# Kernel tuning notes

Hardware: AMD Instinct MI355X
Metric: run time of the kernel (lower is better)

The kernel has to match this reference:

```python
import jax, jax.numpy as jnp
import numpy as np

B, S, D = 4, 4096, 64   # batch, seq_len, input_size
H, HD = 4, 16           # num_heads, head_dim


def setup_inputs() -> dict:
    key = jax.random.key(0)
    ks = jax.random.split(key, 9)
    sd = 1.0 / np.sqrt(D)          # torch Linear default uniform(-1/sqrt(fan_in), ...)
    so = 1.0 / np.sqrt(H * HD)
    u = lambda k, shape, s: jax.random.uniform(k, shape, jnp.float32, -s, s)
    return {
        "x": jax.random.normal(ks[0], (B, S, D), jnp.float32),
        "Wq": u(ks[1], (H, D, HD), sd), "bq": u(ks[2], (H, HD), sd),
        "Wk": u(ks[3], (H, D, HD), sd), "bk": u(ks[4], (H, HD), sd),
        "Wv": u(ks[5], (H, D, HD), sd), "bv": u(ks[6], (H, HD), sd),
        "Wo": u(ks[7], (H * HD, D), so), "bo": u(ks[8], (D,), so),
    }


def reference(x, Wq, bq, Wk, bk, Wv, bv, Wo, bo):
    # Batched per-head projections (fuses the original per-head Linear loop)
    q = jnp.einsum('bsd,hde->bhse', x, Wq) + bq[None, :, None, :]
    k = jnp.einsum('bsd,hde->bhse', x, Wk) + bk[None, :, None, :]
    v = jnp.einsum('bsd,hde->bhse', x, Wv) + bv[None, :, None, :]
    # scores: [B, H, S(query), S(key)]
    scores = jnp.einsum('bhse,bhte->bhst', q, k) / np.sqrt(HD).astype(np.float32)
    # FAITHFUL quirk: torch Softmax(dim=1) on [B,S,S] normalizes over the QUERY axis
    w = jax.nn.softmax(scores, axis=2)
    attended = jnp.einsum('bhst,bhte->bhse', w, v)          # [B,H,S,HD]
    concat = attended.transpose(0, 2, 1, 3).reshape(B, S, H * HD)
    out = concat @ Wo + bo                                   # [B,S,D]
    # FAITHFUL quirk: final softmax over the sequence axis (dim=1)
    return jax.nn.softmax(out, axis=1)
```

## Files before the change

### kernel.cpp

```cpp
#include <hip/hip_runtime.h>
#include <hip/hip_bf16.h>


#define BB 4
#define SS 4096
#define DD 64
#define HH 4
#define HDD 16

typedef unsigned int u32;
typedef unsigned short u16;
typedef __attribute__((ext_vector_type(8))) short bfrag;
typedef __attribute__((ext_vector_type(4))) float floatx4;
typedef __attribute__((ext_vector_type(16))) float floatx16;
typedef __attribute__((ext_vector_type(2))) u32 u32x2;
typedef __attribute__((ext_vector_type(4))) u32 u32x4;

#define LOG2E 1.4426950408889634074f
#define QSCALE (LOG2E * 0.25f)

__device__ __forceinline__ float fexp2(float x) {
#if __has_builtin(__builtin_amdgcn_exp2f)
  return __builtin_amdgcn_exp2f(x);
#else
  float r; asm("v_exp_f32 %0, %1" : "=v"(r) : "v"(x)); return r;
#endif
}
__device__ __forceinline__ float frcp(float x) {
#if __has_builtin(__builtin_amdgcn_rcpf)
  return __builtin_amdgcn_rcpf(x);
#else
  float r; asm("v_rcp_f32 %0, %1" : "=v"(r) : "v"(x)); return r;
#endif
}

__device__ __forceinline__ u16 f2bf(float f) {
  u32 u = __builtin_bit_cast(u32, f);
  return (u16)((u + 0x7FFFu + ((u >> 16) & 1u)) >> 16);
}
__device__ __forceinline__ u32 pack_bf(float lo, float hi) {
#if __has_builtin(__builtin_amdgcn_perm)
  return __builtin_amdgcn_perm(__builtin_bit_cast(u32, hi),
                               __builtin_bit_cast(u32, lo), 0x07060302u);
#else
  u32 a = __builtin_bit_cast(u32, lo);
  u32 b = __builtin_bit_cast(u32, hi);
  return (a >> 16) | (b & 0xFFFF0000u);
#endif
}

__global__ __launch_bounds__(256) void k_proj(
    const float* __restrict__ x,
    const float* __restrict__ Wq, const float* __restrict__ bq,
    const float* __restrict__ Wk, const float* __restrict__ bk,
    const float* __restrict__ Wv, const float* __restrict__ bv,
    u16* __restrict__ qb, u16* __restrict__ kb, float* __restrict__ vf)
{
  __shared__ float xs[16 * 64];
  const int tid = threadIdx.x;
  const int blk = blockIdx.x;
  const int b   = blk >> 8;
  const int s0  = (blk & 255) << 4;
  ((float4*)xs)[tid] = ((const float4*)(x + ((size_t)b * SS + s0) * DD))[tid];
  __syncthreads();

  const int col = tid & 63, h = col >> 4, e = col & 15;
  const int rg  = tid >> 6;
  float aq[4] = {0,0,0,0}, ak[4] = {0,0,0,0}, av[4] = {0,0,0,0};
  const int wofs = h * (DD * HDD) + e;
#pragma unroll 4
  for (int d = 0; d < DD; ++d) {
    float wq = Wq[wofs + d * HDD];
    float wk = Wk[wofs + d * HDD];
    float wv = Wv[wofs + d * HDD];
    const float* xr = xs + (rg * 4) * 64 + d;
#pragma unroll
    for (int r = 0; r < 4; ++r) {
      float xv = xr[r * 64];
      aq[r] += xv * wq; ak[r] += xv * wk; av[r] += xv * wv;
    }
  }
  const float bqv = bq[col], bkv = bk[col], bvv = bv[col];
  size_t base = ((size_t)(b * HH + h) * SS + (s0 + rg * 4)) * HDD + e;
#pragma unroll
  for (int r = 0; r < 4; ++r) {
    qb[base + r * HDD] = f2bf((aq[r] + bqv) * QSCALE);
    kb[base + r * HDD] = f2bf(ak[r] + bkv);
    vf[base + r * HDD] = av[r] + bvv;
  }
}

__global__ __launch_bounds__(256, 8) void k_colsum(
    const u16* __restrict__ qb, const u16* __restrict__ kb,
    float* __restrict__ csp)
{
  const int tid = threadIdx.x;
  const int lane = tid & 63, w = tid >> 6;
  const int l31 = lane & 31, hl = lane >> 5;
  const int bh = blockIdx.z, chunk = blockIdx.y;
  const int t0 = blockIdx.x * 128 + w * 32;
  const size_t base = (size_t)bh * (SS * HDD);

  const bfrag kf = *(const bfrag*)(kb + base + (size_t)(t0 + l31) * HDD + hl * 8);
  const u16* qp = qb + base + (size_t)l31 * HDD + hl * 8;
  const floatx16 z16 = {0.f};
  float c0 = 0.f, c1 = 0.f, c2 = 0.f, c3 = 0.f;
  const int s0 = chunk * 1024;
#pragma unroll 2
  for (int s = s0; s < s0 + 1024; s += 32) {
    bfrag qfr = *(const bfrag*)(qp + (size_t)s * HDD);
    floatx16 d = __builtin_amdgcn_mfma_f32_32x32x16_bf16(qfr, kf, z16, 0, 0, 0);
#pragma unroll
    for (int i = 0; i < 4; ++i) {
      c0 += fexp2(d[4 * i + 0]);
      c1 += fexp2(d[4 * i + 1]);
      c2 += fexp2(d[4 * i + 2]);
      c3 += fexp2(d[4 * i + 3]);
    }
  }
  float c = (c0 + c1) + (c2 + c3);
  c += __shfl_xor(c, 32, 64);
  if (hl == 0)
    csp[((size_t)bh * 4 + chunk) * SS + t0 + l31] = c;
}

__global__ __launch_bounds__(256, 8) void k_attn(
    const u16* __restrict__ qb, const u16* __restrict__ kb,
    const float* __restrict__ vf, const float* __restrict__ csp,
    float* __restrict__ attp)
{
  __shared__ __align__(16) u16 vls[16][264];
  const int tid  = threadIdx.x;
  const int lane = tid & 63, w = tid >> 6;
  const int l31 = lane & 31, hl = lane >> 5;
  const int bh = blockIdx.z, b = bh >> 2, h = bh & 3;
  const int tq = blockIdx.y;
  const int s0 = blockIdx.x * 128 + w * 32;
  const size_t base = (size_t)bh * (SS * HDD);
  const int tbq = tq * 1024;

  const bfrag qf = *(const bfrag*)(qb + base + (size_t)(s0 + l31) * HDD + hl * 8);
  const u16* kp = kb + base + (size_t)l31 * HDD + hl * 8;
  const floatx16 z16 = {0.f};
  floatx16 acc = {0.f};

  const float4* vsrc = (const float4*)(vf + base + (size_t)tbq * HDD);
  const float* cspb = csp + (size_t)bh * 4 * SS + tbq;

#pragma unroll
  for (int ch = 0; ch < 4; ++ch) {
    __syncthreads();
#pragma unroll
    for (int kk = 0; kk < 4; ++kk) {
      int c = kk * 256 + tid;
      int tl = c >> 2, g = c & 3;
      float4 vv = vsrc[ch * 1024 + c];
      const float* cp = cspb + ch * 256 + tl;
      float rc = frcp(cp[0] + cp[SS] + cp[2 * SS] + cp[3 * SS]);
      int i5 = tl >> 5, t5 = tl & 31;
      int sub = ((t5 >> 2) & 1) * 16 + ((t5 >> 3) << 2) + (t5 & 3);
      u16* wp = &vls[0][0] + i5 * 32 + sub;
      wp[(4 * g + 0) * 264] = f2bf(vv.x * rc);
      wp[(4 * g + 1) * 264] = f2bf(vv.y * rc);
      wp[(4 * g + 2) * 264] = f2bf(vv.z * rc);
      wp[(4 * g + 3) * 264] = f2bf(vv.w * rc);
    }
    __syncthreads();

    const u16* vrow = &vls[0][0] + (l31 & 15) * 264 + hl * 16;
    const int tb = tbq + ch * 256;
#pragma unroll 2
    for (int it = 0; it < 8; ++it) {
      bfrag kf = *(const bfrag*)(kp + (size_t)(tb + it * 32) * HDD);
      floatx16 d = __builtin_amdgcn_mfma_f32_32x32x16_bf16(kf, qf, z16, 0, 0, 0);
      u32 wr[8];
#pragma unroll
      for (int p = 0; p < 8; ++p)
        wr[p] = pack_bf(fexp2(d[2 * p]), fexp2(d[2 * p + 1]));
      const u16* va = vrow + it * 32;
      u32x4 af0 = *(const u32x4*)(va);
      u32x4 af1 = *(const u32x4*)(va + 8);
      u32x4 ef0 = {wr[0], wr[1], wr[2], wr[3]};
      u32x4 ef1 = {wr[4], wr[5], wr[6], wr[7]};
      acc = __builtin_amdgcn_mfma_f32_32x32x16_bf16(
          __builtin_bit_cast(bfrag, af0), __builtin_bit_cast(bfrag, ef0), acc, 0, 0, 0);
      acc = __builtin_amdgcn_mfma_f32_32x32x16_bf16(
          __builtin_bit_cast(bfrag, af1), __builtin_bit_cast(bfrag, ef1), acc, 0, 0, 0);
    }
  }

  float* ao = attp + (((size_t)tq * BB + b) * SS + s0 + l31) * (HH * HDD)
            + h * HDD + 4 * hl;
  float4 lo4 = {acc[0], acc[1], acc[2], acc[3]};
  float4 hi4 = {acc[4], acc[5], acc[6], acc[7]};
  *(float4*)ao       = lo4;
  *(float4*)(ao + 8) = hi4;
}

__global__ __launch_bounds__(256) void k_oproj(
    const float* __restrict__ att, const float* __restrict__ Wo,
    const float* __restrict__ bo, float* __restrict__ outp,
    float* __restrict__ part)
{
  __shared__ float wols[64 * 64];
  __shared__ float red[4][64];
  const int tid = threadIdx.x;
  const int blk = blockIdx.x;
  const int b = blk >> 9, s0 = (blk & 511) << 3;
#pragma unroll
  for (int i = 0; i < 4; ++i)
    ((float4*)wols)[tid + 256 * i] = ((const float4*)Wo)[tid + 256 * i];
  __syncthreads();

  const int d = tid & 63, sg = tid >> 6;
  const float bov = bo[d];
  const size_t so = (size_t)BB * SS * 16;
  float es = 0.f;
#pragma unroll
  for (int r = 0; r < 2; ++r) {
    int s = s0 + sg * 2 + r;
    const floatx4* row = (const floatx4*)(att + ((size_t)b * SS + s) * 64);
    float acc = bov;
#pragma unroll
    for (int j = 0; j < 16; ++j) {
      floatx4 c = (row[j] + row[j + so]) + (row[j + 2 * so] + row[j + 3 * so]);
      acc += c[0] * wols[(4*j+0)*64 + d] + c[1] * wols[(4*j+1)*64 + d]
           + c[2] * wols[(4*j+2)*64 + d] + c[3] * wols[(4*j+3)*64 + d];
    }
    outp[((size_t)b * SS + s) * 64 + d] = acc;
    es += fexp2(acc * LOG2E);
  }
  red[sg][d] = es;
  __syncthreads();
  if (tid < 64)
    part[((size_t)b * 512 + (blk & 511)) * 64 + tid] =
        red[0][tid] + red[1][tid] + red[2][tid] + red[3][tid];
}

__global__ __launch_bounds__(256) void k_softmax(
    const float* __restrict__ outp, const float* __restrict__ part,
    float* __restrict__ out)
{
  __shared__ float red[4][64];
  __shared__ float rs[64];
  const int tid = threadIdx.x, d = tid & 63, sg = tid >> 6;
  const int st = blockIdx.x;
  const int b = blockIdx.y;
  {
    float e = 0.f;
    const float* pp = part + ((size_t)b * 512 + sg * 128) * 64 + d;
#pragma unroll 8
    for (int c = 0; c < 128; ++c) e += pp[c * 64];
    red[sg][d] = e;
  }
  __syncthreads();
  if (tid < 64)
    rs[tid] = frcp(red[0][tid] + red[1][tid] + red[2][tid] + red[3][tid]);
  __syncthreads();
  const float r = rs[d];
  const size_t rowbase = ((size_t)b * SS + st * 64 + sg * 16) * 64 + d;
#pragma unroll 4
  for (int i = 0; i < 16; ++i)
    out[rowbase + i * 64] = fexp2(outp[rowbase + i * 64] * LOG2E) * r;
}

extern "C" void kernel_launch(void* const* d_in, const int* in_sizes, int n_in,
                              void* d_out, int out_size, void* d_ws, size_t ws_size,
                              hipStream_t stream) {
  const float* x  = (const float*)d_in[0];
  const float* Wq = (const float*)d_in[1];
  const float* bq = (const float*)d_in[2];
  const float* Wk = (const float*)d_in[3];
  const float* bk = (const float*)d_in[4];
  const float* Wv = (const float*)d_in[5];
  const float* bv = (const float*)d_in[6];
  const float* Wo = (const float*)d_in[7];
  const float* bo = (const float*)d_in[8];

  char* ws = (char*)d_ws;
  constexpr size_t QB_OFF  = 0;
  constexpr size_t KB_OFF  = (size_t)2  << 20;
  constexpr size_t VF_OFF  = (size_t)4  << 20;
  constexpr size_t CSP_OFF = (size_t)10 << 20;
  constexpr size_t ATT_OFF = (size_t)11 << 20;
  constexpr size_t OUT_OFF = (size_t)27 << 20;
  constexpr size_t PT_OFF  = (size_t)31 << 20;

  u16*   qb   = (u16*)  (ws + QB_OFF);
  u16*   kb   = (u16*)  (ws + KB_OFF);
  float* vf   = (float*)(ws + VF_OFF);
  float* csp  = (float*)(ws + CSP_OFF);
  float* attp = (float*)(ws + ATT_OFF);
  float* outp = (float*)(ws + OUT_OFF);
  float* part = (float*)(ws + PT_OFF);
  float* out  = (float*)d_out;

  hipLaunchKernelGGL(k_proj,    dim3(1024),       dim3(256), 0, stream,
                     x, Wq, bq, Wk, bk, Wv, bv, qb, kb, vf);
  hipLaunchKernelGGL(k_colsum,  dim3(32, 4, 16),  dim3(256), 0, stream, qb, kb, csp);
  hipLaunchKernelGGL(k_attn,    dim3(32, 4, 16),  dim3(256), 0, stream,
                     qb, kb, vf, csp, attp);
  hipLaunchKernelGGL(k_oproj,   dim3(2048),       dim3(256), 0, stream,
                     attp, Wo, bo, outp, part);
  hipLaunchKernelGGL(k_softmax, dim3(64, 4),      dim3(256), 0, stream, outp, part, out);
}
```

Baseline: 209.3 us.

## Double-buffer V staging in LDS and prefetch next chunk during MFMA loop

The attention kernel now keeps two LDS buffers for the scaled V tile. It issues global loads for the next chunk's V and column-sum reciprocals before the MFMA loop and writes them to the alternate buffer afterwards, which drops one barrier per chunk. Each thread also now handles a whole key row: one reciprocal computation and four float4 loads, instead of four reciprocals for scattered rows. This aims to hide global load latency behind compute, at the cost of more LDS (which may limit occupancy at 8 blocks/CU) and more live registers for the prefetched data.

```diff
diff --git a/kernel.cpp b/kernel.cpp
--- a/kernel.cpp
+++ b/kernel.cpp
@@ -129,7 +129,7 @@
     const float* __restrict__ vf, const float* __restrict__ csp,
     float* __restrict__ attp)
 {
-  __shared__ __align__(16) u16 vls[16][264];
+  __shared__ __align__(16) u16 vls[2][16][264];
   const int tid  = threadIdx.x;
   const int lane = tid & 63, w = tid >> 6;
   const int l31 = lane & 31, hl = lane >> 5;
@@ -147,27 +147,39 @@
   const float4* vsrc = (const float4*)(vf + base + (size_t)tbq * HDD);
   const float* cspb = csp + (size_t)bh * 4 * SS + tbq;
 
+  const int t5 = tid & 31, i5 = tid >> 5;
+  const int sub = ((t5 >> 2) & 1) * 16 + ((t5 >> 3) << 2) + (t5 & 3);
+  const int wcol = i5 * 32 + sub;
+
+  float4 pv[4];
+  float rc;
+  {
+    const float* cp = cspb + tid;
+    rc = frcp(cp[0] + cp[SS] + cp[2 * SS] + cp[3 * SS]);
+#pragma unroll
+    for (int g = 0; g < 4; ++g) pv[g] = vsrc[tid * 4 + g];
+    u16* wp = &vls[0][0][0] + wcol;
+#pragma unroll
+    for (int g = 0; g < 4; ++g) {
+      wp[(4 * g + 0) * 264] = f2bf(pv[g].x * rc);
+      wp[(4 * g + 1) * 264] = f2bf(pv[g].y * rc);
+      wp[(4 * g + 2) * 264] = f2bf(pv[g].z * rc);
+      wp[(4 * g + 3) * 264] = f2bf(pv[g].w * rc);
+    }
+  }
+  __syncthreads();
+
 #pragma unroll
   for (int ch = 0; ch < 4; ++ch) {
-    __syncthreads();
-#pragma unroll
-    for (int kk = 0; kk < 4; ++kk) {
-      int c = kk * 256 + tid;
-      int tl = c >> 2, g = c & 3;
-      float4 vv = vsrc[ch * 1024 + c];
-      const float* cp = cspb + ch * 256 + tl;
-      float rc = frcp(cp[0] + cp[SS] + cp[2 * SS] + cp[3 * SS]);
-      int i5 = tl >> 5, t5 = tl & 31;
-      int sub = ((t5 >> 2) & 1) * 16 + ((t5 >> 3) << 2) + (t5 & 3);
-      u16* wp = &vls[0][0] + i5 * 32 + sub;
-      wp[(4 * g + 0) * 264] = f2bf(vv.x * rc);
-      wp[(4 * g + 1) * 264] = f2bf(vv.y * rc);
-      wp[(4 * g + 2) * 264] = f2bf(vv.z * rc);
-      wp[(4 * g + 3) * 264] = f2bf(vv.w * rc);
-    }
-    __syncthreads();
-
-    const u16* vrow = &vls[0][0] + (l31 & 15) * 264 + hl * 16;
+    if (ch < 3) {
+      const float* cp = cspb + (ch + 1) * 256 + tid;
+      rc = frcp(cp[0] + cp[SS] + cp[2 * SS] + cp[3 * SS]);
+#pragma unroll
+      for (int g = 0; g < 4; ++g)
+        pv[g] = vsrc[(ch + 1) * 1024 + tid * 4 + g];
+    }
+
+    const u16* vrow = &vls[ch & 1][0][0] + (l31 & 15) * 264 + hl * 16;
     const int tb = tbq + ch * 256;
 #pragma unroll 2
     for (int it = 0; it < 8; ++it) {
@@ -187,6 +199,18 @@
       acc = __builtin_amdgcn_mfma_f32_32x32x16_bf16(
           __builtin_bit_cast(bfrag, af1), __builtin_bit_cast(bfrag, ef1), acc, 0, 0, 0);
     }
+
+    if (ch < 3) {
+      u16* wp = &vls[(ch + 1) & 1][0][0] + wcol;
+#pragma unroll
+      for (int g = 0; g < 4; ++g) {
+        wp[(4 * g + 0) * 264] = f2bf(pv[g].x * rc);
+        wp[(4 * g + 1) * 264] = f2bf(pv[g].y * rc);
+        wp[(4 * g + 2) * 264] = f2bf(pv[g].z * rc);
+        wp[(4 * g + 3) * 264] = f2bf(pv[g].w * rc);
+      }
+    }
+    __syncthreads();
   }
 
   float* ao = attp + (((size_t)tq * BB + b) * SS + s0 + l31) * (HH * HDD)
```

Result: no change. 211.8 us (+1.2%).

## Precompute bf16 transposed V and fold column-sum normalizer into MFMA accumulator

Applied to the files above, without the earlier changes.

Adds a k_prep kernel that converts V to bf16 in the permuted transposed layout once and computes -log2 of the per-key column sums. k_attn then seeds the score MFMA accumulator with that negative log, so exp2 yields already-normalized weights. It reads V straight from global memory instead of rebuilding a scaled LDS tile per chunk, which removes the __syncthreads, LDS traffic and redundant reciprocal work. The cost is an extra kernel launch and extra global reads of the normalizer per iteration. Normalized weights now go through bf16 instead of V*rc, which may slightly change rounding.

```diff
diff --git a/kernel.cpp b/kernel.cpp
--- a/kernel.cpp
+++ b/kernel.cpp
@@ -31,6 +31,13 @@
   return __builtin_amdgcn_rcpf(x);
 #else
   float r; asm("v_rcp_f32 %0, %1" : "=v"(r) : "v"(x)); return r;
+#endif
+}
+__device__ __forceinline__ float flog2(float x) {
+#if __has_builtin(__builtin_amdgcn_logf)
+  return __builtin_amdgcn_logf(x);
+#else
+  return __builtin_log2f(x);
 #endif
 }
 
@@ -124,12 +131,51 @@
     csp[((size_t)bh * 4 + chunk) * SS + t0 + l31] = c;
 }
 
+__global__ __launch_bounds__(256) void k_prep(
+    const float* __restrict__ vf, const float* __restrict__ csp,
+    u16* __restrict__ vt, float* __restrict__ nlcs)
+{
+  __shared__ u16 tile[16][264];
+  const int tid = threadIdx.x;
+  const int bh  = blockIdx.y;
+  const int t0  = blockIdx.x << 8;
+
+  {
+    const float* cp = csp + (size_t)bh * 4 * SS + t0 + tid;
+    float s = (cp[0] + cp[SS]) + (cp[2 * SS] + cp[3 * SS]);
+    nlcs[(size_t)bh * SS + t0 + tid] = -flog2(s);
+  }
+
+  {
+    const int t5 = tid & 31, i5 = tid >> 5;
+    const int sub = ((t5 >> 2) & 1) * 16 + ((t5 >> 3) << 2) + (t5 & 3);
+    const int wcol = i5 * 32 + sub;
+    const floatx4* vsrc = (const floatx4*)(vf + ((size_t)bh * SS + t0 + tid) * HDD);
+#pragma unroll
+    for (int g = 0; g < 4; ++g) {
+      floatx4 vv = vsrc[g];
+      tile[4 * g + 0][wcol] = f2bf(vv[0]);
+      tile[4 * g + 1][wcol] = f2bf(vv[1]);
+      tile[4 * g + 2][wcol] = f2bf(vv[2]);
+      tile[4 * g + 3][wcol] = f2bf(vv[3]);
+    }
+  }
+  __syncthreads();
+
+  {
+    const int row = tid >> 4, seg = tid & 15;
+    const u32x4* src = (const u32x4*)(&tile[row][seg * 16]);
+    u32x4* dst = (u32x4*)(vt + ((size_t)bh * HDD + row) * SS + t0 + seg * 16);
+    dst[0] = src[0];
+    dst[1] = src[1];
+  }
+}
+
 __global__ __launch_bounds__(256, 8) void k_attn(
     const u16* __restrict__ qb, const u16* __restrict__ kb,
-    const float* __restrict__ vf, const float* __restrict__ csp,
+    const u16* __restrict__ vt, const float* __restrict__ nlcs,
     float* __restrict__ attp)
 {
-  __shared__ __align__(16) u16 vls[16][264];
   const int tid  = threadIdx.x;
   const int lane = tid & 63, w = tid >> 6;
   const int l31 = lane & 31, hl = lane >> 5;
@@ -140,53 +186,34 @@
   const int tbq = tq * 1024;
 
   const bfrag qf = *(const bfrag*)(qb + base + (size_t)(s0 + l31) * HDD + hl * 8);
-  const u16* kp = kb + base + (size_t)l31 * HDD + hl * 8;
-  const floatx16 z16 = {0.f};
+  const u16* kp = kb + base + (size_t)(tbq + l31) * HDD + hl * 8;
+  const u16* vrow = vt + ((size_t)bh * HDD + (l31 & 15)) * SS + tbq + hl * 16;
+  const float4* np4 = (const float4*)(nlcs + (size_t)bh * SS + tbq + 4 * hl);
+
   floatx16 acc = {0.f};
 
-  const float4* vsrc = (const float4*)(vf + base + (size_t)tbq * HDD);
-  const float* cspb = csp + (size_t)bh * 4 * SS + tbq;
-
-#pragma unroll
-  for (int ch = 0; ch < 4; ++ch) {
-    __syncthreads();
-#pragma unroll
-    for (int kk = 0; kk < 4; ++kk) {
-      int c = kk * 256 + tid;
-      int tl = c >> 2, g = c & 3;
-      float4 vv = vsrc[ch * 1024 + c];
-      const float* cp = cspb + ch * 256 + tl;
-      float rc = frcp(cp[0] + cp[SS] + cp[2 * SS] + cp[3 * SS]);
-      int i5 = tl >> 5, t5 = tl & 31;
-      int sub = ((t5 >> 2) & 1) * 16 + ((t5 >> 3) << 2) + (t5 & 3);
-      u16* wp = &vls[0][0] + i5 * 32 + sub;
-      wp[(4 * g + 0) * 264] = f2bf(vv.x * rc);
-      wp[(4 * g + 1) * 264] = f2bf(vv.y * rc);
-      wp[(4 * g + 2) * 264] = f2bf(vv.z * rc);
-      wp[(4 * g + 3) * 264] = f2bf(vv.w * rc);
-    }
-    __syncthreads();
-
-    const u16* vrow = &vls[0][0] + (l31 & 15) * 264 + hl * 16;
-    const int tb = tbq + ch * 256;
 #pragma unroll 2
-    for (int it = 0; it < 8; ++it) {
-      bfrag kf = *(const bfrag*)(kp + (size_t)(tb + it * 32) * HDD);
-      floatx16 d = __builtin_amdgcn_mfma_f32_32x32x16_bf16(kf, qf, z16, 0, 0, 0);
-      u32 wr[8];
-#pragma unroll
-      for (int p = 0; p < 8; ++p)
-        wr[p] = pack_bf(fexp2(d[2 * p]), fexp2(d[2 * p + 1]));
-      const u16* va = vrow + it * 32;
-      u32x4 af0 = *(const u32x4*)(va);
-      u32x4 af1 = *(const u32x4*)(va + 8);
-      u32x4 ef0 = {wr[0], wr[1], wr[2], wr[3]};
-      u32x4 ef1 = {wr[4], wr[5], wr[6], wr[7]};
-      acc = __builtin_amdgcn_mfma_f32_32x32x16_bf16(
-          __builtin_bit_cast(bfrag, af0), __builtin_bit_cast(bfrag, ef0), acc, 0, 0, 0);
-      acc = __builtin_amdgcn_mfma_f32_32x32x16_bf16(
-          __builtin_bit_cast(bfrag, af1), __builtin_bit_cast(bfrag, ef1), acc, 0, 0, 0);
-    }
+  for (int it = 0; it < 32; ++it) {
+    float4 n0 = np4[it * 8 + 0];
+    float4 n1 = np4[it * 8 + 2];
+    float4 n2 = np4[it * 8 + 4];
+    float4 n3 = np4[it * 8 + 6];
+    floatx16 cc = {n0.x, n0.y, n0.z, n0.w, n1.x, n1.y, n1.z, n1.w,
+                   n2.x, n2.y, n2.z, n2.w, n3.x, n3.y, n3.z, n3.w};
+    bfrag kf = *(const bfrag*)(kp + (size_t)(it * 32) * HDD);
+    floatx16 d = __builtin_amdgcn_mfma_f32_32x32x16_bf16(kf, qf, cc, 0, 0, 0);
+    u32 wr[8];
+#pragma unroll
+    for (int p = 0; p < 8; ++p)
+      wr[p] = pack_bf(fexp2(d[2 * p]), fexp2(d[2 * p + 1]));
+    u32x4 af0 = *(const u32x4*)(vrow + it * 32);
+    u32x4 af1 = *(const u32x4*)(vrow + it * 32 + 8);
+    u32x4 ef0 = {wr[0], wr[1], wr[2], wr[3]};
+    u32x4 ef1 = {wr[4], wr[5], wr[6], wr[7]};
+    acc = __builtin_amdgcn_mfma_f32_32x32x16_bf16(
+        __builtin_bit_cast(bfrag, af0), __builtin_bit_cast(bfrag, ef0), acc, 0, 0, 0);
+    acc = __builtin_amdgcn_mfma_f32_32x32x16_bf16(
+        __builtin_bit_cast(bfrag, af1), __builtin_bit_cast(bfrag, ef1), acc, 0, 0, 0);
   }
 
   float* ao = attp + (((size_t)tq * BB + b) * SS + s0 + l31) * (HH * HDD)
@@ -281,15 +308,19 @@
   constexpr size_t QB_OFF  = 0;
   constexpr size_t KB_OFF  = (size_t)2  << 20;
   constexpr size_t VF_OFF  = (size_t)4  << 20;
+  constexpr size_t VT_OFF  = (size_t)8  << 20;
   constexpr size_t CSP_OFF = (size_t)10 << 20;
-  constexpr size_t ATT_OFF = (size_t)11 << 20;
-  constexpr size_t OUT_OFF = (size_t)27 << 20;
-  constexpr size_t PT_OFF  = (size_t)31 << 20;
+  constexpr size_t NL_OFF  = (size_t)11 << 20;
+  constexpr size_t ATT_OFF = (size_t)12 << 20;
+  constexpr size_t OUT_OFF = (size_t)28 << 20;
+  constexpr size_t PT_OFF  = (size_t)32 << 20;
 
   u16*   qb   = (u16*)  (ws + QB_OFF);
   u16*   kb   = (u16*)  (ws + KB_OFF);
   float* vf   = (float*)(ws + VF_OFF);
+  u16*   vt   = (u16*)  (ws + VT_OFF);
   float* csp  = (float*)(ws + CSP_OFF);
+  float* nlcs = (float*)(ws + NL_OFF);
   float* attp = (float*)(ws + ATT_OFF);
   float* outp = (float*)(ws + OUT_OFF);
   float* part = (float*)(ws + PT_OFF);
@@ -298,8 +329,10 @@
   hipLaunchKernelGGL(k_proj,    dim3(1024),       dim3(256), 0, stream,
                      x, Wq, bq, Wk, bk, Wv, bv, qb, kb, vf);
   hipLaunchKernelGGL(k_colsum,  dim3(32, 4, 16),  dim3(256), 0, stream, qb, kb, csp);
+  hipLaunchKernelGGL(k_prep,    dim3(16, 16),     dim3(256), 0, stream,
+                     vf, csp, vt, nlcs);
   hipLaunchKernelGGL(k_attn,    dim3(32, 4, 16),  dim3(256), 0, stream,
-                     qb, kb, vf, csp, attp);
+                     qb, kb, vt, nlcs, attp);
   hipLaunchKernelGGL(k_oproj,   dim3(2048),       dim3(256), 0, stream,
                      attp, Wo, bo, outp, part);
   hipLaunchKernelGGL(k_softmax, dim3(64, 4),      dim3(256), 0, stream, outp, part, out);
```

After: 292.2 us. +39.6%, slower.
